# Kernel tuning notes

Hardware: AMD Instinct MI355X
Metric: run time of the kernel (lower is better)

## Reference

```python
import jax, jax.numpy as jnp
import numpy as np

NSLICES = 4
HID = 512
IN_FEAT = 342   # input_shape - 1 (last column is phase)
OUT = 311
BATCH = 256


def cubic(y0, y1, y2, y3, mu):
    # Catmull-Rom cubic interpolation, as in the original PFNN code
    return (
        (-0.5 * y0 + 1.5 * y1 - 1.5 * y2 + 0.5 * y3) * mu * mu * mu
        + (y0 - 2.5 * y1 + 2.0 * y2 - 0.5 * y3) * mu * mu
        + (-0.5 * y0 + 0.5 * y2) * mu
        + y1
    )


def setup_inputs() -> dict:
    key = jax.random.key(0)
    ks = jax.random.split(key, 7)
    x = jax.random.uniform(ks[0], (BATCH, IN_FEAT + 1), dtype=jnp.float32)
    s = 0.02
    W0 = jax.random.normal(ks[1], (NSLICES, HID, IN_FEAT), dtype=jnp.float32) * s
    b0 = jax.random.normal(ks[2], (NSLICES, HID), dtype=jnp.float32) * s
    W1 = jax.random.normal(ks[3], (NSLICES, HID, HID), dtype=jnp.float32) * s
    b1 = jax.random.normal(ks[4], (NSLICES, HID), dtype=jnp.float32) * s
    W2 = jax.random.normal(ks[5], (NSLICES, OUT, HID), dtype=jnp.float32) * s
    b2 = jax.random.normal(ks[6], (NSLICES, OUT), dtype=jnp.float32) * s
    return {"x": x, "W0": W0, "b0": b0, "W1": W1, "b1": b1, "W2": W2, "b2": b2}


def reference(x, W0, b0, W1, b1, W2, b2):
    phase = x[:, -1]                       # [B]
    pscale = NSLICES * phase
    mu = jnp.mod(pscale, 1.0)              # [B]
    i1 = jnp.floor(pscale).astype(jnp.int32) % NSLICES
    i0 = (i1 - 1) % NSLICES
    i2 = (i1 + 1) % NSLICES
    i3 = (i1 + 2) % NSLICES
    muW = mu[:, None, None]                # broadcast over (out, in)
    mub = mu[:, None]

    Wb0 = cubic(W0[i0], W0[i1], W0[i2], W0[i3], muW)   # [B, 512, 342]
    bb0 = cubic(b0[i0], b0[i1], b0[i2], b0[i3], mub)   # [B, 512]
    Wb1 = cubic(W1[i0], W1[i1], W1[i2], W1[i3], muW)   # [B, 512, 512]
    bb1 = cubic(b1[i0], b1[i1], b1[i2], b1[i3], mub)
    Wb2 = cubic(W2[i0], W2[i1], W2[i2], W2[i3], muW)   # [B, 311, 512]
    bb2 = cubic(b2[i0], b2[i1], b2[i2], b2[i3], mub)

    h = x[:, :-1]                                       # [B, 342]
    h = jax.nn.elu(jnp.einsum('boi,bi->bo', Wb0, h) + bb0)
    h = jax.nn.elu(jnp.einsum('boi,bi->bo', Wb1, h) + bb1)
    out = jnp.einsum('boi,bi->bo', Wb2, h) + bb2        # [B, 311]
    return out
```

## Files before the change

### kernel.cpp

```cpp
#include <hip/hip_runtime.h>
#include <math.h>

#define HID 512
#define IN_FEAT 342
#define OUTD 311
#define BATCH 256
#define KP0 352
#define MP2 320
#define XROW (IN_FEAT + 1)

typedef unsigned short u16;
typedef short bf16x8 __attribute__((ext_vector_type(8)));
typedef float f32x4 __attribute__((ext_vector_type(4)));

__device__ __forceinline__ u16 f2bf_rne(float v) {
    unsigned int x = __float_as_uint(v);
    unsigned int r = (x + 0x7fffu + ((x >> 16) & 1u)) >> 16;
    return (u16)r;
}
__device__ __forceinline__ float bf2f(u16 u) {
    return __uint_as_float(((unsigned int)u) << 16);
}

__device__ __forceinline__ void split8(const float* __restrict__ src, bf16x8& hi, bf16x8& lo) {
#pragma unroll
    for (int j = 0; j < 8; j++) {
        u16 h = f2bf_rne(src[j]);
        hi[j] = (short)h;
        lo[j] = (short)f2bf_rne(src[j] - bf2f(h));
    }
}

template<int KP, int KLDS, int NB, int FINAL, int MODE, int KW, int MW, int NBY>
__global__ __launch_bounds__(NB * 16, 1) void layer_f32w(
    const float* __restrict__ W,
    const float* __restrict__ x,
    const u16* __restrict__ Hhi, const u16* __restrict__ Hlo,
    const float* __restrict__ bias, int Mb,
    u16* __restrict__ Ohi, u16* __restrict__ Olo, float* __restrict__ outp)
{
    constexpr int NTHR = NB * 16;
    union SharedU {
        u16 h[2][NB * KLDS];
        float acc[4][NB][17];
    };
    __shared__ SharedU sm;

    const int blk = (int)blockIdx.x;
    const int bx = (blk >> 3) & 7;
    const int by = (blk & 7) | ((blk >> 6) << 3);
    if (by >= NBY) return;

    const int tid = (int)threadIdx.x;
    const int b0 = bx * NB;
    const int o0 = by * 16;

    constexpr int CH = KP / 8;
    if constexpr (MODE == 0) {
        for (int idx = tid; idx < NB * CH; idx += NTHR) {
            int r = idx / CH, c = idx - r * CH;
            int k = c * 8;
            const float* xr = x + (size_t)(b0 + r) * XROW;
            float src[8];
#pragma unroll
            for (int j = 0; j < 8; j++) {
                int kk = k + j;
                src[j] = (kk < IN_FEAT) ? xr[kk] : 0.f;
            }
            bf16x8 hi, lo;
            split8(src, hi, lo);
            *reinterpret_cast<bf16x8*>(&sm.h[0][r * KLDS + k]) = hi;
            *reinterpret_cast<bf16x8*>(&sm.h[1][r * KLDS + k]) = lo;
        }
    } else {
        for (int idx = tid; idx < NB * CH; idx += NTHR) {
            int r = idx / CH, c = idx - r * CH;
            size_t g = (size_t)(b0 + r) * KP + c * 8;
            *reinterpret_cast<uint4*>(&sm.h[0][r * KLDS + c * 8]) =
                *reinterpret_cast<const uint4*>(Hhi + g);
            *reinterpret_cast<uint4*>(&sm.h[1][r * KLDS + c * 8]) =
                *reinterpret_cast<const uint4*>(Hlo + g);
        }
    }
    __syncthreads();

    const int lane = tid & 63;
    const int w = tid >> 6;
    const int s = w & 3;
    const int t = w >> 2;
    const int m = lane & 15;
    const int q = lane >> 4;

    const int orow = o0 + m;
    const bool vrow = (MW == HID) ? true : (orow < MW);
    const float* wr = W + ((size_t)s * MW + (vrow ? orow : 0)) * KW;
    const u16* hp = &sm.h[0][(t * 16 + m) * KLDS + q * 8];

    const int brow = b0 + t * 16 + m;
    const float ps = 4.f * x[(size_t)brow * XROW + IN_FEAT];
    const float fl = floorf(ps);
    const float mu = ps - fl;
    const int i1 = ((int)fl) & 3;
    const int jj = (s - i1) & 3;
    const float mu2 = mu * mu, mu3 = mu2 * mu;
    const float ds = (jj == 0) ? ( 1.5f * mu3 - 2.5f * mu2 + 1.0f)
                   : (jj == 1) ? (-1.5f * mu3 + 2.0f * mu2 + 0.5f * mu)
                   : (jj == 2) ? ( 0.5f * mu3 - 0.5f * mu2)
                   :             (-0.5f * mu3 + mu2 - 0.5f * mu);

    f32x4 a0 = {0.f, 0.f, 0.f, 0.f};
    f32x4 a1 = {0.f, 0.f, 0.f, 0.f};
    f32x4 a2 = {0.f, 0.f, 0.f, 0.f};
#pragma unroll
    for (int cc = 0; cc < KP / 32; ++cc) {
        const int k0 = cc * 32 + q * 8;
        float ws[8];
        if (vrow && (cc * 32 + 32 <= KW)) {
            if constexpr (KW % 4 == 0) {
                const float4* p = reinterpret_cast<const float4*>(wr + k0);
                float4 v0 = p[0], v1 = p[1];
                ws[0] = v0.x; ws[1] = v0.y; ws[2] = v0.z; ws[3] = v0.w;
                ws[4] = v1.x; ws[5] = v1.y; ws[6] = v1.z; ws[7] = v1.w;
            } else {
                const float2* p = reinterpret_cast<const float2*>(wr + k0);
                float2 v0 = p[0], v1 = p[1], v2 = p[2], v3 = p[3];
                ws[0] = v0.x; ws[1] = v0.y; ws[2] = v1.x; ws[3] = v1.y;
                ws[4] = v2.x; ws[5] = v2.y; ws[6] = v3.x; ws[7] = v3.y;
            }
        } else {
#pragma unroll
            for (int j = 0; j < 8; j++) {
                int kk = k0 + j;
                ws[j] = (vrow && kk < KW) ? wr[kk] : 0.f;
            }
        }
        bf16x8 ah, al;
        split8(ws, ah, al);
        bf16x8 bh = *reinterpret_cast<const bf16x8*>(hp + cc * 32);
        bf16x8 bl = *reinterpret_cast<const bf16x8*>(hp + cc * 32 + NB * KLDS);
        a0 = __builtin_amdgcn_mfma_f32_16x16x32_bf16(ah, bh, a0, 0, 0, 0);
        a1 = __builtin_amdgcn_mfma_f32_16x16x32_bf16(ah, bl, a1, 0, 0, 0);
        a2 = __builtin_amdgcn_mfma_f32_16x16x32_bf16(al, bh, a2, 0, 0, 0);
    }
    __syncthreads();

    f32x4 sum = a0 + a1 + a2;
#pragma unroll
    for (int r = 0; r < 4; ++r) {
        int o = o0 + q * 4 + r;
        float bb = (o < Mb) ? bias[(size_t)s * Mb + o] : 0.f;
        sm.acc[s][t * 16 + m][q * 4 + r] = ds * (sum[r] + bb);
    }
    __syncthreads();

    const int b_l = tid >> 4;
    const int o_l = tid & 15;
    float vv = sm.acc[0][b_l][o_l] + sm.acc[1][b_l][o_l]
             + sm.acc[2][b_l][o_l] + sm.acc[3][b_l][o_l];
    const int o = o0 + o_l;
    const int b = b0 + b_l;
    if (!FINAL) {
        float e = (vv > 0.f) ? vv : expm1f(vv);
        u16 h = f2bf_rne(e);
        Ohi[(size_t)b * HID + o] = h;
        Olo[(size_t)b * HID + o] = f2bf_rne(e - bf2f(h));
    } else if (o < OUTD) {
        outp[(size_t)b * OUTD + o] = vv;
    }
}

extern "C" void kernel_launch(void* const* d_in, const int* in_sizes, int n_in,
                              void* d_out, int out_size, void* d_ws, size_t ws_size,
                              hipStream_t stream) {
    const float* x  = (const float*)d_in[0];
    const float* W0 = (const float*)d_in[1];
    const float* b0v = (const float*)d_in[2];
    const float* W1 = (const float*)d_in[3];
    const float* b1v = (const float*)d_in[4];
    const float* W2 = (const float*)d_in[5];
    const float* b2v = (const float*)d_in[6];
    float* out = (float*)d_out;

    char* pw = (char*)d_ws;
    auto alloc = [&](size_t bytes) { char* r = pw; pw += (bytes + 255) & ~(size_t)255; return r; };

    u16* hahi = (u16*)alloc((size_t)BATCH * HID * 2);
    u16* halo = (u16*)alloc((size_t)BATCH * HID * 2);
    u16* hbhi = (u16*)alloc((size_t)BATCH * HID * 2);
    u16* hblo = (u16*)alloc((size_t)BATCH * HID * 2);

    layer_f32w<KP0, 360, 32, 0, 0, IN_FEAT, HID, 32><<<256, 512, 0, stream>>>(
        W0, x, nullptr, nullptr, b0v, HID, hahi, halo, nullptr);

    layer_f32w<HID, 520, 32, 0, 1, HID, HID, 32><<<256, 512, 0, stream>>>(
        W1, x, hahi, halo, b1v, HID, hbhi, hblo, nullptr);

    layer_f32w<HID, 520, 32, 1, 1, HID, OUTD, 20><<<192, 512, 0, stream>>>(
        W2, x, hbhi, hblo, b2v, OUTD, nullptr, nullptr, out);
}
```

Baseline: 103.6 us.

## Fuse three layer kernels into one persistent kernel with grid barriers

Merges the three per-layer launches into a single persistent kernel where each block runs all three layer phases, separated by atomic-counter grid barriers in workspace memory, plus a small kernel to zero the counters. This removes inter-kernel launch gaps and tail effects between layers. It relies on all 256 blocks being co-resident, and the barrier has a spin timeout that could silently break ordering if they are not.

Result: slower. 127.5 us (+23.0%).

```diff
diff --git a/kernel.cpp b/kernel.cpp
--- a/kernel.cpp
+++ b/kernel.cpp
@@ -6,8 +6,10 @@
 #define OUTD 311
 #define BATCH 256
 #define KP0 352
-#define MP2 320
 #define XROW (IN_FEAT + 1)
+#define NB 32
+#define NTHR 512
+#define NBLK 256
 
 typedef unsigned short u16;
 typedef short bf16x8 __attribute__((ext_vector_type(8)));
@@ -31,29 +33,44 @@
     }
 }
 
-template<int KP, int KLDS, int NB, int FINAL, int MODE, int KW, int MW, int NBY>
-__global__ __launch_bounds__(NB * 16, 1) void layer_f32w(
-    const float* __restrict__ W,
-    const float* __restrict__ x,
+struct Params {
+    const float *x, *W0, *b0, *W1, *b1, *W2, *b2;
+    u16 *hahi, *halo, *hbhi, *hblo;
+    unsigned* bar;
+    float* outp;
+};
+
+union SharedU {
+    u16 h[2][NB * 520];
+    float acc[4][NB][17];
+};
+
+__device__ __forceinline__ void gbar(unsigned* cnt, unsigned nblk) {
+    __syncthreads();
+    if (threadIdx.x == 0) {
+        __builtin_amdgcn_fence(__ATOMIC_RELEASE, "agent");
+        __hip_atomic_fetch_add(cnt, 1u, __ATOMIC_RELAXED, __HIP_MEMORY_SCOPE_AGENT);
+        long spins = 0;
+        while (__hip_atomic_load(cnt, __ATOMIC_RELAXED, __HIP_MEMORY_SCOPE_AGENT) < nblk) {
+            __builtin_amdgcn_s_sleep(2);
+            if (++spins > (1L << 26)) break;
+        }
+        __builtin_amdgcn_fence(__ATOMIC_ACQUIRE, "agent");
+    }
+    __syncthreads();
+}
+
+template<int KP, int KLDS, int MODE, int KW, int MW, int FINAL>
+__device__ __forceinline__ void phase(SharedU& sm, int bx, int by, int tid,
+    const float* __restrict__ W, const float* __restrict__ x,
     const u16* __restrict__ Hhi, const u16* __restrict__ Hlo,
     const float* __restrict__ bias, int Mb,
     u16* __restrict__ Ohi, u16* __restrict__ Olo, float* __restrict__ outp)
 {
-    constexpr int NTHR = NB * 16;
-    union SharedU {
-        u16 h[2][NB * KLDS];
-        float acc[4][NB][17];
-    };
-    __shared__ SharedU sm;
-
-    const int blk = (int)blockIdx.x;
-    const int bx = (blk >> 3) & 7;
-    const int by = (blk & 7) | ((blk >> 6) << 3);
-    if (by >= NBY) return;
-
-    const int tid = (int)threadIdx.x;
     const int b0 = bx * NB;
     const int o0 = by * 16;
+    u16* h0 = &sm.h[0][0];
+    u16* h1 = &sm.h[1][0];
 
     constexpr int CH = KP / 8;
     if constexpr (MODE == 0) {
@@ -69,16 +86,16 @@
             }
             bf16x8 hi, lo;
             split8(src, hi, lo);
-            *reinterpret_cast<bf16x8*>(&sm.h[0][r * KLDS + k]) = hi;
-            *reinterpret_cast<bf16x8*>(&sm.h[1][r * KLDS + k]) = lo;
+            *reinterpret_cast<bf16x8*>(&h0[r * KLDS + k]) = hi;
+            *reinterpret_cast<bf16x8*>(&h1[r * KLDS + k]) = lo;
         }
     } else {
         for (int idx = tid; idx < NB * CH; idx += NTHR) {
             int r = idx / CH, c = idx - r * CH;
             size_t g = (size_t)(b0 + r) * KP + c * 8;
-            *reinterpret_cast<uint4*>(&sm.h[0][r * KLDS + c * 8]) =
+            *reinterpret_cast<uint4*>(&h0[r * KLDS + c * 8]) =
                 *reinterpret_cast<const uint4*>(Hhi + g);
-            *reinterpret_cast<uint4*>(&sm.h[1][r * KLDS + c * 8]) =
+            *reinterpret_cast<uint4*>(&h1[r * KLDS + c * 8]) =
                 *reinterpret_cast<const uint4*>(Hlo + g);
         }
     }
@@ -94,7 +111,8 @@
     const int orow = o0 + m;
     const bool vrow = (MW == HID) ? true : (orow < MW);
     const float* wr = W + ((size_t)s * MW + (vrow ? orow : 0)) * KW;
-    const u16* hp = &sm.h[0][(t * 16 + m) * KLDS + q * 8];
+    const u16* hp = &h0[(t * 16 + m) * KLDS + q * 8];
+    const u16* hpl = &h1[(t * 16 + m) * KLDS + q * 8];
 
     const int brow = b0 + t * 16 + m;
     const float ps = 4.f * x[(size_t)brow * XROW + IN_FEAT];
@@ -117,13 +135,13 @@
         float ws[8];
         if (vrow && (cc * 32 + 32 <= KW)) {
             if constexpr (KW % 4 == 0) {
-                const float4* p = reinterpret_cast<const float4*>(wr + k0);
-                float4 v0 = p[0], v1 = p[1];
+                const float4* p4 = reinterpret_cast<const float4*>(wr + k0);
+                float4 v0 = p4[0], v1 = p4[1];
                 ws[0] = v0.x; ws[1] = v0.y; ws[2] = v0.z; ws[3] = v0.w;
                 ws[4] = v1.x; ws[5] = v1.y; ws[6] = v1.z; ws[7] = v1.w;
             } else {
-                const float2* p = reinterpret_cast<const float2*>(wr + k0);
-                float2 v0 = p[0], v1 = p[1], v2 = p[2], v3 = p[3];
+                const float2* p2 = reinterpret_cast<const float2*>(wr + k0);
+                float2 v0 = p2[0], v1 = p2[1], v2 = p2[2], v3 = p2[3];
                 ws[0] = v0.x; ws[1] = v0.y; ws[2] = v1.x; ws[3] = v1.y;
                 ws[4] = v2.x; ws[5] = v2.y; ws[6] = v3.x; ws[7] = v3.y;
             }
@@ -137,7 +155,7 @@
         bf16x8 ah, al;
         split8(ws, ah, al);
         bf16x8 bh = *reinterpret_cast<const bf16x8*>(hp + cc * 32);
-        bf16x8 bl = *reinterpret_cast<const bf16x8*>(hp + cc * 32 + NB * KLDS);
+        bf16x8 bl = *reinterpret_cast<const bf16x8*>(hpl + cc * 32);
         a0 = __builtin_amdgcn_mfma_f32_16x16x32_bf16(ah, bh, a0, 0, 0, 0);
         a1 = __builtin_amdgcn_mfma_f32_16x16x32_bf16(ah, bl, a1, 0, 0, 0);
         a2 = __builtin_amdgcn_mfma_f32_16x16x32_bf16(al, bh, a2, 0, 0, 0);
@@ -169,32 +187,53 @@
     }
 }
 
+__global__ void zero_bar(unsigned* bar) {
+    if (threadIdx.x < 128) bar[threadIdx.x] = 0u;
+}
+
+__global__ __launch_bounds__(NTHR, 1) void fused3(Params p) {
+    __shared__ SharedU sm;
+    const int blk = (int)blockIdx.x;
+    const int tid = (int)threadIdx.x;
+    const int bx = (blk >> 3) & 7;
+    const int by = (blk & 7) | ((blk >> 6) << 3);
+
+    phase<KP0, 360, 0, IN_FEAT, HID, 0>(sm, bx, by, tid,
+        p.W0, p.x, nullptr, nullptr, p.b0, HID, p.hahi, p.halo, nullptr);
+    gbar(p.bar + 0, NBLK);
+
+    phase<HID, 520, 1, HID, HID, 0>(sm, bx, by, tid,
+        p.W1, p.x, p.hahi, p.halo, p.b1, HID, p.hbhi, p.hblo, nullptr);
+    gbar(p.bar + 64, NBLK);
+
+    if (by < 20) {
+        phase<HID, 520, 1, HID, OUTD, 1>(sm, bx, by, tid,
+            p.W2, p.x, p.hbhi, p.hblo, p.b2, OUTD, nullptr, nullptr, p.outp);
+    }
+}
+
 extern "C" void kernel_launch(void* const* d_in, const int* in_sizes, int n_in,
                               void* d_out, int out_size, void* d_ws, size_t ws_size,
                               hipStream_t stream) {
-    const float* x  = (const float*)d_in[0];
-    const float* W0 = (const float*)d_in[1];
-    const float* b0v = (const float*)d_in[2];
-    const float* W1 = (const float*)d_in[3];
-    const float* b1v = (const float*)d_in[4];
-    const float* W2 = (const float*)d_in[5];
-    const float* b2v = (const float*)d_in[6];
-    float* out = (float*)d_out;
+    Params p;
+    p.x  = (const float*)d_in[0];
+    p.W0 = (const float*)d_in[1];
+    p.b0 = (const float*)d_in[2];
+    p.W1 = (const float*)d_in[3];
+    p.b1 = (const float*)d_in[4];
+    p.W2 = (const float*)d_in[5];
+    p.b2 = (const float*)d_in[6];
+    p.outp = (float*)d_out;
 
     char* pw = (char*)d_ws;
     auto alloc = [&](size_t bytes) { char* r = pw; pw += (bytes + 255) & ~(size_t)255; return r; };
 
-    u16* hahi = (u16*)alloc((size_t)BATCH * HID * 2);
-    u16* halo = (u16*)alloc((size_t)BATCH * HID * 2);
-    u16* hbhi = (u16*)alloc((size_t)BATCH * HID * 2);
-    u16* hblo = (u16*)alloc((size_t)BATCH * HID * 2);
-
-    layer_f32w<KP0, 360, 32, 0, 0, IN_FEAT, HID, 32><<<256, 512, 0, stream>>>(
-        W0, x, nullptr, nullptr, b0v, HID, hahi, halo, nullptr);
-
-    layer_f32w<HID, 520, 32, 0, 1, HID, HID, 32><<<256, 512, 0, stream>>>(
-        W1, x, hahi, halo, b1v, HID, hbhi, hblo, nullptr);
-
-    layer_f32w<HID, 520, 32, 1, 1, HID, OUTD, 20><<<192, 512, 0, stream>>>(
-        W2, x, hbhi, hblo, b2v, OUTD, nullptr, nullptr, out);
-}
+    p.bar  = (unsigned*)alloc(512);
+    p.hahi = (u16*)alloc((size_t)BATCH * HID * 2);
+    p.halo = (u16*)alloc((size_t)BATCH * HID * 2);
+    p.hbhi = (u16*)alloc((size_t)BATCH * HID * 2);
+    p.hblo = (u16*)alloc((size_t)BATCH * HID * 2);
+
+    zero_bar<<<1, 128, 0, stream>>>(p.bar);
+    fused3<<<NBLK, NTHR, 0, stream>>>(p);
+}
```

## Prefetch weight rows into registers and warm L2 with later-layer weights

Applied to the files above, without the earlier changes.

Each thread now loads its whole weight row slice into registers before the activation staging and barrier, so the global loads overlap the LDS fill instead of sitting inside the MFMA loop. The first-layer kernel also reads all of W1 and W2 once and keeps a dummy sum alive through an empty asm statement, so those weights are in L2/MALL when the next kernels run. Launch bounds change to allow two blocks per CU. The cost is much higher register pressure and extra memory traffic in layer 0.

After: 113.1 us. 1.09x slower.

```diff
diff --git a/kernel.cpp b/kernel.cpp
--- a/kernel.cpp
+++ b/kernel.cpp
@@ -6,8 +6,9 @@
 #define OUTD 311
 #define BATCH 256
 #define KP0 352
-#define MP2 320
 #define XROW (IN_FEAT + 1)
+#define NB 32
+#define NTHR 512
 
 typedef unsigned short u16;
 typedef short bf16x8 __attribute__((ext_vector_type(8)));
@@ -31,15 +32,14 @@
     }
 }
 
-template<int KP, int KLDS, int NB, int FINAL, int MODE, int KW, int MW, int NBY>
-__global__ __launch_bounds__(NB * 16, 1) void layer_f32w(
-    const float* __restrict__ W,
-    const float* __restrict__ x,
+template<int KP, int KLDS, int FINAL, int MODE, int KW, int MW, int NBY, int WARM>
+__global__ __launch_bounds__(NTHR, 2) void layer_pf(
+    const float* __restrict__ W, const float* __restrict__ x,
     const u16* __restrict__ Hhi, const u16* __restrict__ Hlo,
     const float* __restrict__ bias, int Mb,
-    u16* __restrict__ Ohi, u16* __restrict__ Olo, float* __restrict__ outp)
+    u16* __restrict__ Ohi, u16* __restrict__ Olo, float* __restrict__ outp,
+    const float* __restrict__ Wa, const float* __restrict__ Wb, int nbf4)
 {
-    constexpr int NTHR = NB * 16;
     union SharedU {
         u16 h[2][NB * KLDS];
         float acc[4][NB][17];
@@ -52,8 +52,59 @@
     if (by >= NBY) return;
 
     const int tid = (int)threadIdx.x;
+    const int lane = tid & 63;
+    const int w = tid >> 6;
+    const int s = w & 3;
+    const int t = w >> 2;
+    const int m = lane & 15;
+    const int q = lane >> 4;
     const int b0 = bx * NB;
     const int o0 = by * 16;
+
+    const int orow = o0 + m;
+    const bool vrow = (MW == HID) ? true : (orow < MW);
+    const float* wr = W + ((size_t)s * MW + (vrow ? orow : 0)) * KW;
+
+    constexpr int NCC = KP / 32;
+    constexpr int CCF = KW / 32;
+
+    float4 wv4[(KW % 4 == 0) ? 2 * CCF : 1];
+    float2 wv2[(KW % 4 == 0) ? 1 : 4 * CCF];
+    float wtail[8];
+    if constexpr (KW % 4 == 0) {
+        const float4* p4 = reinterpret_cast<const float4*>(wr + q * 8);
+#pragma unroll
+        for (int cc = 0; cc < CCF; ++cc) {
+            wv4[2 * cc]     = p4[cc * 8];
+            wv4[2 * cc + 1] = p4[cc * 8 + 1];
+        }
+    } else {
+        const float2* p2 = reinterpret_cast<const float2*>(wr + q * 8);
+#pragma unroll
+        for (int cc = 0; cc < CCF; ++cc) {
+#pragma unroll
+            for (int j = 0; j < 4; ++j) wv2[4 * cc + j] = p2[cc * 16 + j];
+        }
+#pragma unroll
+        for (int j = 0; j < 8; ++j) {
+            int kk = CCF * 32 + q * 8 + j;
+            wtail[j] = (kk < KW) ? wr[kk] : 0.f;
+        }
+    }
+
+    float wsum = 0.f;
+    if constexpr (WARM) {
+        const float4* wa = reinterpret_cast<const float4*>(Wa);
+        const float4* wb = reinterpret_cast<const float4*>(Wb);
+        int gi = blk * NTHR + tid;
+        float4 t0 = wa[gi];
+        float4 t1 = wa[gi + 131072];
+        float4 t2 = wb[gi];
+        int gi2 = (gi + 131072 < nbf4) ? gi + 131072 : gi;
+        float4 t3 = wb[gi2];
+        wsum = t0.x + t0.y + t0.z + t0.w + t1.x + t1.y + t1.z + t1.w
+             + t2.x + t2.y + t2.z + t2.w + t3.x + t3.y + t3.z + t3.w;
+    }
 
     constexpr int CH = KP / 8;
     if constexpr (MODE == 0) {
@@ -84,17 +135,8 @@
     }
     __syncthreads();
 
-    const int lane = tid & 63;
-    const int w = tid >> 6;
-    const int s = w & 3;
-    const int t = w >> 2;
-    const int m = lane & 15;
-    const int q = lane >> 4;
-
-    const int orow = o0 + m;
-    const bool vrow = (MW == HID) ? true : (orow < MW);
-    const float* wr = W + ((size_t)s * MW + (vrow ? orow : 0)) * KW;
-    const u16* hp = &sm.h[0][(t * 16 + m) * KLDS + q * 8];
+    const u16* hp  = &sm.h[0][(t * 16 + m) * KLDS + q * 8];
+    const u16* hpl = &sm.h[1][(t * 16 + m) * KLDS + q * 8];
 
     const int brow = b0 + t * 16 + m;
     const float ps = 4.f * x[(size_t)brow * XROW + IN_FEAT];
@@ -112,32 +154,25 @@
     f32x4 a1 = {0.f, 0.f, 0.f, 0.f};
     f32x4 a2 = {0.f, 0.f, 0.f, 0.f};
 #pragma unroll
-    for (int cc = 0; cc < KP / 32; ++cc) {
-        const int k0 = cc * 32 + q * 8;
+    for (int cc = 0; cc < NCC; ++cc) {
         float ws[8];
-        if (vrow && (cc * 32 + 32 <= KW)) {
-            if constexpr (KW % 4 == 0) {
-                const float4* p = reinterpret_cast<const float4*>(wr + k0);
-                float4 v0 = p[0], v1 = p[1];
-                ws[0] = v0.x; ws[1] = v0.y; ws[2] = v0.z; ws[3] = v0.w;
-                ws[4] = v1.x; ws[5] = v1.y; ws[6] = v1.z; ws[7] = v1.w;
-            } else {
-                const float2* p = reinterpret_cast<const float2*>(wr + k0);
-                float2 v0 = p[0], v1 = p[1], v2 = p[2], v3 = p[3];
-                ws[0] = v0.x; ws[1] = v0.y; ws[2] = v1.x; ws[3] = v1.y;
-                ws[4] = v2.x; ws[5] = v2.y; ws[6] = v3.x; ws[7] = v3.y;
-            }
+        if constexpr (KW % 4 == 0) {
+            float4 v0 = wv4[2 * cc], v1 = wv4[2 * cc + 1];
+            ws[0] = v0.x; ws[1] = v0.y; ws[2] = v0.z; ws[3] = v0.w;
+            ws[4] = v1.x; ws[5] = v1.y; ws[6] = v1.z; ws[7] = v1.w;
+        } else if (cc < CCF) {
+            float2 v0 = wv2[4 * cc], v1 = wv2[4 * cc + 1];
+            float2 v2 = wv2[4 * cc + 2], v3 = wv2[4 * cc + 3];
+            ws[0] = v0.x; ws[1] = v0.y; ws[2] = v1.x; ws[3] = v1.y;
+            ws[4] = v2.x; ws[5] = v2.y; ws[6] = v3.x; ws[7] = v3.y;
         } else {
 #pragma unroll
-            for (int j = 0; j < 8; j++) {
-                int kk = k0 + j;
-                ws[j] = (vrow && kk < KW) ? wr[kk] : 0.f;
-            }
+            for (int j = 0; j < 8; ++j) ws[j] = wtail[j];
         }
         bf16x8 ah, al;
         split8(ws, ah, al);
         bf16x8 bh = *reinterpret_cast<const bf16x8*>(hp + cc * 32);
-        bf16x8 bl = *reinterpret_cast<const bf16x8*>(hp + cc * 32 + NB * KLDS);
+        bf16x8 bl = *reinterpret_cast<const bf16x8*>(hpl + cc * 32);
         a0 = __builtin_amdgcn_mfma_f32_16x16x32_bf16(ah, bh, a0, 0, 0, 0);
         a1 = __builtin_amdgcn_mfma_f32_16x16x32_bf16(ah, bl, a1, 0, 0, 0);
         a2 = __builtin_amdgcn_mfma_f32_16x16x32_bf16(al, bh, a2, 0, 0, 0);
@@ -167,6 +202,10 @@
     } else if (o < OUTD) {
         outp[(size_t)b * OUTD + o] = vv;
     }
+
+    if constexpr (WARM) {
+        asm volatile("" :: "v"(wsum));
+    }
 }
 
 extern "C" void kernel_launch(void* const* d_in, const int* in_sizes, int n_in,
@@ -189,12 +228,12 @@
     u16* hbhi = (u16*)alloc((size_t)BATCH * HID * 2);
     u16* hblo = (u16*)alloc((size_t)BATCH * HID * 2);
 
-    layer_f32w<KP0, 360, 32, 0, 0, IN_FEAT, HID, 32><<<256, 512, 0, stream>>>(
-        W0, x, nullptr, nullptr, b0v, HID, hahi, halo, nullptr);
-
-    layer_f32w<HID, 520, 32, 0, 1, HID, HID, 32><<<256, 512, 0, stream>>>(
-        W1, x, hahi, halo, b1v, HID, hbhi, hblo, nullptr);
-
-    layer_f32w<HID, 520, 32, 1, 1, HID, OUTD, 20><<<192, 512, 0, stream>>>(
-        W2, x, hbhi, hblo, b2v, OUTD, nullptr, nullptr, out);
-}
+    layer_pf<KP0, 360, 0, 0, IN_FEAT, HID, 32, 1><<<256, NTHR, 0, stream>>>(
+        W0, x, nullptr, nullptr, b0v, HID, hahi, halo, nullptr, W1, W2, 159232);
+
+    layer_pf<HID, 520, 0, 1, HID, HID, 32, 0><<<256, NTHR, 0, stream>>>(
+        W1, x, hahi, halo, b1v, HID, hbhi, hblo, nullptr, nullptr, nullptr, 0);
+
+    layer_pf<HID, 520, 1, 1, HID, OUTD, 20, 0><<<192, NTHR, 0, stream>>>(
+        W2, x, hbhi, hblo, b2v, OUTD, nullptr, nullptr, out, nullptr, nullptr, 0);
+}
```

## Pre-split weights into bf16 hi/lo MFMA fragment layout in a prep kernel

Applied to the files above, without the earlier changes.

Adds a prep kernel that converts the fp32 weights into bf16 hi/lo pairs, stored in the per-lane MFMA fragment order, once per call. The three layer kernels then load ready fragments with contiguous 16-byte loads instead of loading fp32 rows and splitting them in the inner loop. Before, each weight tile was re-read and re-split by all 8 batch-tile blocks; now that conversion is done once. The cost is an extra kernel launch and a write plus re-read of the fragment buffers, which are about the same byte size as the fp32 weights.

After: 99.91 us. 3.6% less time.

```diff
diff --git a/kernel.cpp b/kernel.cpp
--- a/kernel.cpp
+++ b/kernel.cpp
@@ -6,8 +6,21 @@
 #define OUTD 311
 #define BATCH 256
 #define KP0 352
-#define MP2 320
 #define XROW (IN_FEAT + 1)
+#define NB 32
+#define NTHR 512
+
+#define NT0 32
+#define NCC0 11
+#define NT1 32
+#define NCC1 16
+#define NT2 20
+#define NCC2 16
+
+#define P0 (4 * 512 * 44)
+#define P1 (4 * 512 * 64)
+#define P2 (4 * 320 * 64)
+#define PTOT (P0 + P1 + P2)
 
 typedef unsigned short u16;
 typedef short bf16x8 __attribute__((ext_vector_type(8)));
@@ -22,6 +35,8 @@
     return __uint_as_float(((unsigned int)u) << 16);
 }
 
+union U8 { u16 u[8]; uint4 v; };
+
 __device__ __forceinline__ void split8(const float* __restrict__ src, bf16x8& hi, bf16x8& lo) {
 #pragma unroll
     for (int j = 0; j < 8; j++) {
@@ -31,15 +46,82 @@
     }
 }
 
-template<int KP, int KLDS, int NB, int FINAL, int MODE, int KW, int MW, int NBY>
-__global__ __launch_bounds__(NB * 16, 1) void layer_f32w(
-    const float* __restrict__ W,
-    const float* __restrict__ x,
+__global__ __launch_bounds__(256) void prep_frag(
+    const float* __restrict__ W0, const float* __restrict__ W1, const float* __restrict__ W2,
+    u16* __restrict__ F0, u16* __restrict__ F1, u16* __restrict__ F2)
+{
+    int i = blockIdx.x * 256 + threadIdx.x;
+    if (i >= PTOT) return;
+
+    float src[8];
+    u16* dst;
+    if (i < P0) {
+        int s = i / (512 * 44);
+        int rem = i - s * (512 * 44);
+        int row = rem / 44, c = rem - row * 44;
+        int k = c * 8;
+        const float* rp = W0 + ((size_t)s * 512 + row) * IN_FEAT;
+        if (k + 8 <= IN_FEAT) {
+            const float2* p2 = reinterpret_cast<const float2*>(rp + k);
+            float2 v0 = p2[0], v1 = p2[1], v2 = p2[2], v3 = p2[3];
+            src[0] = v0.x; src[1] = v0.y; src[2] = v1.x; src[3] = v1.y;
+            src[4] = v2.x; src[5] = v2.y; src[6] = v3.x; src[7] = v3.y;
+        } else {
+#pragma unroll
+            for (int j = 0; j < 8; j++) src[j] = (k + j < IN_FEAT) ? rp[k + j] : 0.f;
+        }
+        int ot = row >> 4, m = row & 15, cc = c >> 2, q = c & 3;
+        dst = F0 + ((size_t)(s * NT0 + ot) * NCC0 + cc) * 1024 + (q * 16 + m) * 8;
+    } else if (i < P0 + P1) {
+        int l = i - P0;
+        int s = l >> 15;
+        int row = (l >> 6) & 511, c = l & 63;
+        int k = c * 8;
+        const float4* p4 = reinterpret_cast<const float4*>(
+            W1 + ((size_t)s * 512 + row) * 512 + k);
+        float4 v0 = p4[0], v1 = p4[1];
+        src[0] = v0.x; src[1] = v0.y; src[2] = v0.z; src[3] = v0.w;
+        src[4] = v1.x; src[5] = v1.y; src[6] = v1.z; src[7] = v1.w;
+        int ot = row >> 4, m = row & 15, cc = c >> 2, q = c & 3;
+        dst = F1 + ((size_t)(s * NT1 + ot) * NCC1 + cc) * 1024 + (q * 16 + m) * 8;
+    } else {
+        int l = i - P0 - P1;
+        int s = l / (320 * 64);
+        int rem = l - s * (320 * 64);
+        int row = rem >> 6, c = rem & 63;
+        int k = c * 8;
+        if (row < OUTD) {
+            const float4* p4 = reinterpret_cast<const float4*>(
+                W2 + ((size_t)s * OUTD + row) * 512 + k);
+            float4 v0 = p4[0], v1 = p4[1];
+            src[0] = v0.x; src[1] = v0.y; src[2] = v0.z; src[3] = v0.w;
+            src[4] = v1.x; src[5] = v1.y; src[6] = v1.z; src[7] = v1.w;
+        } else {
+#pragma unroll
+            for (int j = 0; j < 8; j++) src[j] = 0.f;
+        }
+        int ot = row >> 4, m = row & 15, cc = c >> 2, q = c & 3;
+        dst = F2 + ((size_t)(s * NT2 + ot) * NCC2 + cc) * 1024 + (q * 16 + m) * 8;
+    }
+
+    U8 hi, lo;
+#pragma unroll
+    for (int j = 0; j < 8; j++) {
+        u16 h = f2bf_rne(src[j]);
+        hi.u[j] = h;
+        lo.u[j] = f2bf_rne(src[j] - bf2f(h));
+    }
+    *reinterpret_cast<uint4*>(dst)       = hi.v;
+    *reinterpret_cast<uint4*>(dst + 512) = lo.v;
+}
+
+template<int KP, int KLDS, int FINAL, int MODE, int NT, int NBY>
+__global__ __launch_bounds__(NTHR, 1) void layer_frag(
+    const u16* __restrict__ Wf, const float* __restrict__ x,
     const u16* __restrict__ Hhi, const u16* __restrict__ Hlo,
     const float* __restrict__ bias, int Mb,
     u16* __restrict__ Ohi, u16* __restrict__ Olo, float* __restrict__ outp)
 {
-    constexpr int NTHR = NB * 16;
     union SharedU {
         u16 h[2][NB * KLDS];
         float acc[4][NB][17];
@@ -91,10 +173,10 @@
     const int m = lane & 15;
     const int q = lane >> 4;
 
-    const int orow = o0 + m;
-    const bool vrow = (MW == HID) ? true : (orow < MW);
-    const float* wr = W + ((size_t)s * MW + (vrow ? orow : 0)) * KW;
-    const u16* hp = &sm.h[0][(t * 16 + m) * KLDS + q * 8];
+    constexpr int NCC = KP / 32;
+    const u16* wf = Wf + ((size_t)(s * NT + by) * NCC) * 1024 + lane * 8;
+    const u16* hp  = &sm.h[0][(t * 16 + m) * KLDS + q * 8];
+    const u16* hpl = &sm.h[1][(t * 16 + m) * KLDS + q * 8];
 
     const int brow = b0 + t * 16 + m;
     const float ps = 4.f * x[(size_t)brow * XROW + IN_FEAT];
@@ -112,32 +194,11 @@
     f32x4 a1 = {0.f, 0.f, 0.f, 0.f};
     f32x4 a2 = {0.f, 0.f, 0.f, 0.f};
 #pragma unroll
-    for (int cc = 0; cc < KP / 32; ++cc) {
-        const int k0 = cc * 32 + q * 8;
-        float ws[8];
-        if (vrow && (cc * 32 + 32 <= KW)) {
-            if constexpr (KW % 4 == 0) {
-                const float4* p = reinterpret_cast<const float4*>(wr + k0);
-                float4 v0 = p[0], v1 = p[1];
-                ws[0] = v0.x; ws[1] = v0.y; ws[2] = v0.z; ws[3] = v0.w;
-                ws[4] = v1.x; ws[5] = v1.y; ws[6] = v1.z; ws[7] = v1.w;
-            } else {
-                const float2* p = reinterpret_cast<const float2*>(wr + k0);
-                float2 v0 = p[0], v1 = p[1], v2 = p[2], v3 = p[3];
-                ws[0] = v0.x; ws[1] = v0.y; ws[2] = v1.x; ws[3] = v1.y;
-                ws[4] = v2.x; ws[5] = v2.y; ws[6] = v3.x; ws[7] = v3.y;
-            }
-        } else {
-#pragma unroll
-            for (int j = 0; j < 8; j++) {
-                int kk = k0 + j;
-                ws[j] = (vrow && kk < KW) ? wr[kk] : 0.f;
-            }
-        }
-        bf16x8 ah, al;
-        split8(ws, ah, al);
+    for (int cc = 0; cc < NCC; ++cc) {
+        bf16x8 ah = *reinterpret_cast<const bf16x8*>(wf + cc * 1024);
+        bf16x8 al = *reinterpret_cast<const bf16x8*>(wf + cc * 1024 + 512);
         bf16x8 bh = *reinterpret_cast<const bf16x8*>(hp + cc * 32);
-        bf16x8 bl = *reinterpret_cast<const bf16x8*>(hp + cc * 32 + NB * KLDS);
+        bf16x8 bl = *reinterpret_cast<const bf16x8*>(hpl + cc * 32);
         a0 = __builtin_amdgcn_mfma_f32_16x16x32_bf16(ah, bh, a0, 0, 0, 0);
         a1 = __builtin_amdgcn_mfma_f32_16x16x32_bf16(ah, bl, a1, 0, 0, 0);
         a2 = __builtin_amdgcn_mfma_f32_16x16x32_bf16(al, bh, a2, 0, 0, 0);
@@ -184,17 +245,22 @@
     char* pw = (char*)d_ws;
     auto alloc = [&](size_t bytes) { char* r = pw; pw += (bytes + 255) & ~(size_t)255; return r; };
 
+    u16* F0 = (u16*)alloc((size_t)4 * NT0 * NCC0 * 1024 * 2);
+    u16* F1 = (u16*)alloc((size_t)4 * NT1 * NCC1 * 1024 * 2);
+    u16* F2 = (u16*)alloc((size_t)4 * NT2 * NCC2 * 1024 * 2);
     u16* hahi = (u16*)alloc((size_t)BATCH * HID * 2);
     u16* halo = (u16*)alloc((size_t)BATCH * HID * 2);
     u16* hbhi = (u16*)alloc((size_t)BATCH * HID * 2);
     u16* hblo = (u16*)alloc((size_t)BATCH * HID * 2);
 
-    layer_f32w<KP0, 360, 32, 0, 0, IN_FEAT, HID, 32><<<256, 512, 0, stream>>>(
-        W0, x, nullptr, nullptr, b0v, HID, hahi, halo, nullptr);
-
-    layer_f32w<HID, 520, 32, 0, 1, HID, HID, 32><<<256, 512, 0, stream>>>(
-        W1, x, hahi, halo, b1v, HID, hbhi, hblo, nullptr);
-
-    layer_f32w<HID, 520, 32, 1, 1, HID, OUTD, 20><<<192, 512, 0, stream>>>(
-        W2, x, hbhi, hblo, b2v, OUTD, nullptr, nullptr, out);
-}
+    prep_frag<<<PTOT / 256, 256, 0, stream>>>(W0, W1, W2, F0, F1, F2);
+
+    layer_frag<KP0, 360, 0, 0, NT0, 32><<<256, NTHR, 0, stream>>>(
+        F0, x, nullptr, nullptr, b0v, HID, hahi, halo, nullptr);
+
+    layer_frag<HID, 520, 0, 1, NT1, 32><<<256, NTHR, 0, stream>>>(
+        F1, x, hahi, halo, b1v, HID, hbhi, hblo, nullptr);
+
+    layer_frag<HID, 520, 1, 1, NT2, 20><<<192, NTHR, 0, stream>>>(
+        F2, x, hbhi, hblo, b2v, OUTD, nullptr, nullptr, out);
+}
```
